# Optimization experiments

Hardware: AMD Instinct MI355X
Metric: run time of the kernel (lower is better)

## Reference

```python
import jax, jax.numpy as jnp
import numpy as np

N_NODES = 100000
N_EDGES = 3200000  # avg degree 32
D_IN = 128
D_OUT = 64
BN_EPS = 0.001


def setup_inputs() -> dict:
    key = jax.random.key(0)
    k1, k2, k3, k4, k5 = jax.random.split(key, 5)
    x = jax.random.normal(k1, (N_NODES, D_IN), dtype=jnp.float32)
    W = jax.random.normal(k2, (D_IN, D_OUT), dtype=jnp.float32) * 0.05
    edge_val = jax.random.uniform(k3, (N_EDGES,), dtype=jnp.float32)
    edge_src = jax.random.randint(k4, (N_EDGES,), 0, N_NODES, dtype=jnp.int32)
    edge_dst = jax.random.randint(k5, (N_EDGES,), 0, N_NODES, dtype=jnp.int32)
    return {"x": x, "W": W, "edge_val": edge_val,
            "edge_src": edge_src, "edge_dst": edge_dst}


def reference(x, W, edge_val, edge_src, edge_dst):
    # pre_sup = X @ W  (dense feature transform; dropout rate is 0 -> identity)
    pre_sup = x @ W  # [N, D_OUT]
    # support = A @ pre_sup, A given in COO form: A[dst, src] = edge_val
    msgs = edge_val[:, None] * pre_sup[edge_src]          # [E, D_OUT]
    out = jax.ops.segment_sum(msgs, edge_dst, num_segments=N_NODES)  # [N, D_OUT]
    # tf.nn.moments over all-but-last axis + batch_norm (no scale/offset, eps=1e-3)
    mean = jnp.mean(out, axis=0)
    var = jnp.var(out, axis=0)
    out = (out - mean) * jax.lax.rsqrt(var + BN_EPS)
    return jax.nn.relu(out)
```

## Files before the change

kernel.cpp:

```cpp
#include <hip/hip_runtime.h>
#include <stdint.h>

#define D_IN  128
#define D_OUT 64
#define BN_EPS 1e-3f

#define BIN_SHIFT 6
#define BIN_NODES 64
#define BIN_CAP   2560
#define CHUNK     8192
#define MAX_BINS  1600

typedef __attribute__((ext_vector_type(8))) short bf16x8;
typedef __attribute__((ext_vector_type(4))) float f32x4;

__device__ __forceinline__ ushort f32_to_bf16_rne(float f) {
  uint u = __float_as_uint(f);
  u += 0x7FFFu + ((u >> 16) & 1u);
  return (ushort)(u >> 16);
}
__device__ __forceinline__ float bf16_to_f32(ushort h) {
  return __uint_as_float((uint)h << 16);
}

__global__ __launch_bounds__(256) void gemm_mfma_kernel(
    const float* __restrict__ x, const float* __restrict__ W,
    ushort* __restrict__ pre16, int n_nodes, int n_tiles) {
  __shared__ ushort Wb[D_IN * D_OUT];
  const int t = threadIdx.x;
  for (int i = t; i < D_IN * D_OUT; i += 256) Wb[i] = f32_to_bf16_rne(W[i]);
  __syncthreads();

  const int lane = t & 63;
  const int wave = t >> 6;
  const int m = lane & 15;
  const int quad = lane >> 4;

  bf16x8 bfrag[4][4];
#pragma unroll
  for (int nt = 0; nt < 4; ++nt)
#pragma unroll
    for (int s = 0; s < 4; ++s)
#pragma unroll
      for (int j = 0; j < 8; ++j)
        bfrag[nt][s][j] =
            (short)Wb[(32 * s + quad * 8 + j) * D_OUT + nt * 16 + m];

  for (int tile = blockIdx.x; tile < n_tiles; tile += gridDim.x) {
    const int rbase = tile * 64 + wave * 16;
    const int row = rbase + m;
    const size_t rl = (size_t)min(row, n_nodes - 1);
    f32x4 acc0 = {0.f, 0.f, 0.f, 0.f}, acc1 = {0.f, 0.f, 0.f, 0.f};
    f32x4 acc2 = {0.f, 0.f, 0.f, 0.f}, acc3 = {0.f, 0.f, 0.f, 0.f};
#pragma unroll
    for (int s = 0; s < 4; ++s) {
      const float4 xa = *(const float4*)&x[rl * D_IN + s * 32 + quad * 8];
      const float4 xb = *(const float4*)&x[rl * D_IN + s * 32 + quad * 8 + 4];
      bf16x8 af;
      af[0] = (short)f32_to_bf16_rne(xa.x);
      af[1] = (short)f32_to_bf16_rne(xa.y);
      af[2] = (short)f32_to_bf16_rne(xa.z);
      af[3] = (short)f32_to_bf16_rne(xa.w);
      af[4] = (short)f32_to_bf16_rne(xb.x);
      af[5] = (short)f32_to_bf16_rne(xb.y);
      af[6] = (short)f32_to_bf16_rne(xb.z);
      af[7] = (short)f32_to_bf16_rne(xb.w);
      acc0 = __builtin_amdgcn_mfma_f32_16x16x32_bf16(af, bfrag[0][s], acc0, 0, 0, 0);
      acc1 = __builtin_amdgcn_mfma_f32_16x16x32_bf16(af, bfrag[1][s], acc1, 0, 0, 0);
      acc2 = __builtin_amdgcn_mfma_f32_16x16x32_bf16(af, bfrag[2][s], acc2, 0, 0, 0);
      acc3 = __builtin_amdgcn_mfma_f32_16x16x32_bf16(af, bfrag[3][s], acc3, 0, 0, 0);
    }
#pragma unroll
    for (int reg = 0; reg < 4; ++reg) {
      const int r = rbase + quad * 4 + reg;
      if (r < n_nodes) {
        ushort* po = &pre16[(size_t)r * D_OUT + m];
        po[0]  = f32_to_bf16_rne(acc0[reg]);
        po[16] = f32_to_bf16_rne(acc1[reg]);
        po[32] = f32_to_bf16_rne(acc2[reg]);
        po[48] = f32_to_bf16_rne(acc3[reg]);
      }
    }
  }
}

__global__ __launch_bounds__(256) void partition_kernel(
    const float* __restrict__ ev, const int* __restrict__ esrc,
    const int* __restrict__ edst, int* __restrict__ bin_cursor,
    uint2* __restrict__ bucket, int n_edges, int n_bins) {
  __shared__ int cnt[MAX_BINS];
  __shared__ int base[MAX_BINS];
  const int t = threadIdx.x;
  const int beg = blockIdx.x * CHUNK;
  const int end = min(beg + CHUNK, n_edges);

  for (int i = t; i < n_bins; i += 256) cnt[i] = 0;
  __syncthreads();

  for (int i = beg + t * 4; i < end; i += 1024) {
    if (i + 3 < end) {
      const int4 d4 = *(const int4*)&edst[i];
      atomicAdd(&cnt[d4.x >> BIN_SHIFT], 1);
      atomicAdd(&cnt[d4.y >> BIN_SHIFT], 1);
      atomicAdd(&cnt[d4.z >> BIN_SHIFT], 1);
      atomicAdd(&cnt[d4.w >> BIN_SHIFT], 1);
    } else {
      for (int k = i; k < end; ++k) atomicAdd(&cnt[edst[k] >> BIN_SHIFT], 1);
    }
  }
  __syncthreads();

  for (int i = t; i < n_bins; i += 256) {
    const int c = cnt[i];
    int b = 0;
    if (c > 0) b = atomicAdd(&bin_cursor[i], c);
    if (b > BIN_CAP) b = BIN_CAP;
    base[i] = i * BIN_CAP + b;
    cnt[i] = 0;
  }
  __syncthreads();

  for (int i = beg + t * 4; i < end; i += 1024) {
    if (i + 3 < end) {
      const int4 d4 = *(const int4*)&edst[i];
      const int4 s4 = *(const int4*)&esrc[i];
      const float4 v4 = *(const float4*)&ev[i];
#pragma unroll
      for (int k = 0; k < 4; ++k) {
        const int dst = (&d4.x)[k];
        const int src = (&s4.x)[k];
        const float v = (&v4.x)[k];
        const int bin = dst >> BIN_SHIFT;
        const int r = atomicAdd(&cnt[bin], 1);
        const int pos = base[bin] + r;
        if (pos < (bin + 1) * BIN_CAP) {
          const uint w0 = ((uint)(dst & (BIN_NODES - 1)) << 17) | (uint)src;
          bucket[pos] = make_uint2(w0, __float_as_uint(v));
        }
      }
    } else {
      for (int k = i; k < end; ++k) {
        const int dst = edst[k];
        const int bin = dst >> BIN_SHIFT;
        const int r = atomicAdd(&cnt[bin], 1);
        const int pos = base[bin] + r;
        if (pos < (bin + 1) * BIN_CAP) {
          const uint w0 = ((uint)(dst & (BIN_NODES - 1)) << 17) | (uint)esrc[k];
          bucket[pos] = make_uint2(w0, __float_as_uint(ev[k]));
        }
      }
    }
  }
}

__global__ __launch_bounds__(256) void bin_sort_gather_kernel(
    const ushort* __restrict__ pre16, const uint2* __restrict__ bucket,
    const int* __restrict__ bin_cursor, float* __restrict__ out,
    float* __restrict__ stats, int n_nodes) {
  __shared__ uint s_src[BIN_CAP];
  __shared__ ushort s_val[BIN_CAP];
  __shared__ int s_hist[BIN_NODES];
  __shared__ int s_off[BIN_NODES + 1];
  __shared__ int s_cur[BIN_NODES];

  const int t = threadIdx.x;
  const int bin = blockIdx.x;
  const int cnt = min(bin_cursor[bin], BIN_CAP);
  const int64_t rbase = (int64_t)bin * BIN_CAP;

  if (t < BIN_NODES) s_hist[t] = 0;
  __syncthreads();

  for (int i = t; i < cnt; i += 256)
    atomicAdd(&s_hist[bucket[rbase + i].x >> 17], 1);
  __syncthreads();

  int own = (t < BIN_NODES) ? s_hist[t] : 0;
  for (int off = 1; off < BIN_NODES; off <<= 1) {
    int u = 0;
    if (t < BIN_NODES && t >= off) u = s_hist[t - off];
    __syncthreads();
    if (t < BIN_NODES) s_hist[t] += u;
    __syncthreads();
  }
  if (t < BIN_NODES) {
    const int e = s_hist[t] - own;
    s_off[t] = e;
    s_cur[t] = e;
  }
  if (t == 0) s_off[BIN_NODES] = cnt;
  __syncthreads();

  for (int i = t; i < cnt; i += 256) {
    const uint2 r = bucket[rbase + i];
    const int d = r.x >> 17;
    const int p = atomicAdd(&s_cur[d], 1);
    s_src[p] = r.x & 0x1FFFFu;
    s_val[p] = f32_to_bf16_rne(__uint_as_float(r.y));
  }
  __syncthreads();

  const int lane = t & 63;
  const int wave = t >> 6;
  const int half = lane >> 5;
  const int hl = lane & 31;
  const int node0 = bin * BIN_NODES;
  float csx = 0.f, csy = 0.f, cs2x = 0.f, cs2y = 0.f;

  for (int nl = wave; nl < BIN_NODES; nl += 4) {
    const int node = node0 + nl;
    if (node < n_nodes) {
      const int jb = s_off[nl], je = s_off[nl + 1];
      float a0x = 0.f, a0y = 0.f, a1x = 0.f, a1y = 0.f;
      float a2x = 0.f, a2y = 0.f, a3x = 0.f, a3y = 0.f;
      float a4x = 0.f, a4y = 0.f, a5x = 0.f, a5y = 0.f;
      float a6x = 0.f, a6y = 0.f, a7x = 0.f, a7y = 0.f;
      int j = jb + half;
      for (; j + 14 < je; j += 16) {
        const uint src0 = s_src[j],      src1 = s_src[j + 2];
        const uint src2 = s_src[j + 4],  src3 = s_src[j + 6];
        const uint src4 = s_src[j + 8],  src5 = s_src[j + 10];
        const uint src6 = s_src[j + 12], src7 = s_src[j + 14];
        const float v0 = bf16_to_f32(s_val[j]);
        const float v1 = bf16_to_f32(s_val[j + 2]);
        const float v2 = bf16_to_f32(s_val[j + 4]);
        const float v3 = bf16_to_f32(s_val[j + 6]);
        const float v4 = bf16_to_f32(s_val[j + 8]);
        const float v5 = bf16_to_f32(s_val[j + 10]);
        const float v6 = bf16_to_f32(s_val[j + 12]);
        const float v7 = bf16_to_f32(s_val[j + 14]);
        const uint p0 = *(const uint*)&pre16[(size_t)src0 * D_OUT + 2 * hl];
        const uint p1 = *(const uint*)&pre16[(size_t)src1 * D_OUT + 2 * hl];
        const uint p2 = *(const uint*)&pre16[(size_t)src2 * D_OUT + 2 * hl];
        const uint p3 = *(const uint*)&pre16[(size_t)src3 * D_OUT + 2 * hl];
        const uint p4 = *(const uint*)&pre16[(size_t)src4 * D_OUT + 2 * hl];
        const uint p5 = *(const uint*)&pre16[(size_t)src5 * D_OUT + 2 * hl];
        const uint p6 = *(const uint*)&pre16[(size_t)src6 * D_OUT + 2 * hl];
        const uint p7 = *(const uint*)&pre16[(size_t)src7 * D_OUT + 2 * hl];
        a0x += v0 * bf16_to_f32((ushort)(p0 & 0xFFFFu));
        a0y += v0 * bf16_to_f32((ushort)(p0 >> 16));
        a1x += v1 * bf16_to_f32((ushort)(p1 & 0xFFFFu));
        a1y += v1 * bf16_to_f32((ushort)(p1 >> 16));
        a2x += v2 * bf16_to_f32((ushort)(p2 & 0xFFFFu));
        a2y += v2 * bf16_to_f32((ushort)(p2 >> 16));
        a3x += v3 * bf16_to_f32((ushort)(p3 & 0xFFFFu));
        a3y += v3 * bf16_to_f32((ushort)(p3 >> 16));
        a4x += v4 * bf16_to_f32((ushort)(p4 & 0xFFFFu));
        a4y += v4 * bf16_to_f32((ushort)(p4 >> 16));
        a5x += v5 * bf16_to_f32((ushort)(p5 & 0xFFFFu));
        a5y += v5 * bf16_to_f32((ushort)(p5 >> 16));
        a6x += v6 * bf16_to_f32((ushort)(p6 & 0xFFFFu));
        a6y += v6 * bf16_to_f32((ushort)(p6 >> 16));
        a7x += v7 * bf16_to_f32((ushort)(p7 & 0xFFFFu));
        a7y += v7 * bf16_to_f32((ushort)(p7 >> 16));
      }
      for (; j + 6 < je; j += 8) {
        const uint src0 = s_src[j],     src1 = s_src[j + 2];
        const uint src2 = s_src[j + 4], src3 = s_src[j + 6];
        const float v0 = bf16_to_f32(s_val[j]);
        const float v1 = bf16_to_f32(s_val[j + 2]);
        const float v2 = bf16_to_f32(s_val[j + 4]);
        const float v3 = bf16_to_f32(s_val[j + 6]);
        const uint p0 = *(const uint*)&pre16[(size_t)src0 * D_OUT + 2 * hl];
        const uint p1 = *(const uint*)&pre16[(size_t)src1 * D_OUT + 2 * hl];
        const uint p2 = *(const uint*)&pre16[(size_t)src2 * D_OUT + 2 * hl];
        const uint p3 = *(const uint*)&pre16[(size_t)src3 * D_OUT + 2 * hl];
        a0x += v0 * bf16_to_f32((ushort)(p0 & 0xFFFFu));
        a0y += v0 * bf16_to_f32((ushort)(p0 >> 16));
        a1x += v1 * bf16_to_f32((ushort)(p1 & 0xFFFFu));
        a1y += v1 * bf16_to_f32((ushort)(p1 >> 16));
        a2x += v2 * bf16_to_f32((ushort)(p2 & 0xFFFFu));
        a2y += v2 * bf16_to_f32((ushort)(p2 >> 16));
        a3x += v3 * bf16_to_f32((ushort)(p3 & 0xFFFFu));
        a3y += v3 * bf16_to_f32((ushort)(p3 >> 16));
      }
      for (; j < je; j += 2) {
        const uint src = s_src[j];
        const float v = bf16_to_f32(s_val[j]);
        const uint p = *(const uint*)&pre16[(size_t)src * D_OUT + 2 * hl];
        a0x += v * bf16_to_f32((ushort)(p & 0xFFFFu));
        a0y += v * bf16_to_f32((ushort)(p >> 16));
      }
      float ax = ((a0x + a1x) + (a2x + a3x)) + ((a4x + a5x) + (a6x + a7x));
      float ay = ((a0y + a1y) + (a2y + a3y)) + ((a4y + a5y) + (a6y + a7y));
      ax += __shfl_xor(ax, 32);
      ay += __shfl_xor(ay, 32);
      if (half == 0) {
        *(float2*)&out[(size_t)node * D_OUT + 2 * hl] = make_float2(ax, ay);
        csx += ax;
        cs2x += ax * ax;
        csy += ay;
        cs2y += ay * ay;
      }
    }
  }
  __syncthreads();

  float* red = (float*)s_src;
  float* red2 = red + 256;
  if (half == 0) {
    red[wave * 64 + 2 * hl] = csx;
    red[wave * 64 + 2 * hl + 1] = csy;
    red2[wave * 64 + 2 * hl] = cs2x;
    red2[wave * 64 + 2 * hl + 1] = cs2y;
  }
  __syncthreads();
  if (t < 64) {
    float s = red[t] + red[64 + t] + red[128 + t] + red[192 + t];
    float s2 = red2[t] + red2[64 + t] + red2[128 + t] + red2[192 + t];
    atomicAdd(&stats[t], s);
    atomicAdd(&stats[64 + t], s2);
  }
}

__global__ __launch_bounds__(256) void norm_kernel(
    float* __restrict__ out, const float* __restrict__ stats, int64_t n_vec4,
    float inv_n) {
  const int c = (threadIdx.x * 4) & 63;
  float mean[4], scale[4];
#pragma unroll
  for (int k = 0; k < 4; ++k) {
    mean[k] = stats[c + k] * inv_n;
    const float var = stats[64 + c + k] * inv_n - mean[k] * mean[k];
    scale[k] = rsqrtf(var + BN_EPS);
  }
  const int64_t stride = (int64_t)gridDim.x * 256;
  for (int64_t i = (int64_t)blockIdx.x * 256 + threadIdx.x; i < n_vec4;
       i += stride) {
    float4 v = ((float4*)out)[i];
    v.x = (v.x - mean[0]) * scale[0];
    v.y = (v.y - mean[1]) * scale[1];
    v.z = (v.z - mean[2]) * scale[2];
    v.w = (v.w - mean[3]) * scale[3];
    v.x = v.x > 0.f ? v.x : 0.f;
    v.y = v.y > 0.f ? v.y : 0.f;
    v.z = v.z > 0.f ? v.z : 0.f;
    v.w = v.w > 0.f ? v.w : 0.f;
    ((float4*)out)[i] = v;
  }
}

extern "C" void kernel_launch(void* const* d_in, const int* in_sizes, int n_in,
                              void* d_out, int out_size, void* d_ws,
                              size_t ws_size, hipStream_t stream) {
  const float* x = (const float*)d_in[0];
  const float* W = (const float*)d_in[1];
  const float* ev = (const float*)d_in[2];
  const int* esrc = (const int*)d_in[3];
  const int* edst = (const int*)d_in[4];

  const int n_nodes = in_sizes[0] / D_IN;
  const int n_edges = in_sizes[2];
  const int64_t n_out = (int64_t)n_nodes * D_OUT;
  const int n_bins = (n_nodes + BIN_NODES - 1) >> BIN_SHIFT;
  const int n_row_tiles = (n_nodes + 63) / 64;

  float* out = (float*)d_out;

  char* w = (char*)d_ws;
  ushort* pre16 = (ushort*)w;             w += (size_t)n_nodes * D_OUT * 2;
  int* bin_cursor = (int*)w;              w += (size_t)n_bins * 4;
  float* stats = (float*)w;               w += 128 * 4;
  w = (char*)(((uintptr_t)w + 7) & ~(uintptr_t)7);
  uint2* bucket = (uint2*)w;

  hipMemsetAsync(bin_cursor, 0, (size_t)n_bins * 4, stream);
  hipMemsetAsync(stats, 0, 128 * 4, stream);

  gemm_mfma_kernel<<<(n_row_tiles + 1) / 2, 256, 0, stream>>>(
      x, W, pre16, n_nodes, n_row_tiles);
  partition_kernel<<<(n_edges + CHUNK - 1) / CHUNK, 256, 0, stream>>>(
      ev, esrc, edst, bin_cursor, bucket, n_edges, n_bins);
  bin_sort_gather_kernel<<<n_bins, 256, 0, stream>>>(pre16, bucket, bin_cursor,
                                                     out, stats, n_nodes);
  norm_kernel<<<2048, 256, 0, stream>>>(out, stats, n_out / 4,
                                        1.0f / (float)n_nodes);
}
```

Before: 312.2 us.

## Split fused bin-sort/gather into separate kernels with per-node wave parallelism

The fused per-bin sort+gather kernel becomes two kernels. A bin sort kernel writes the sorted (src, val) records back to global memory along with per-node segment bounds. A gather kernel then uses one wave per node across many more blocks. BN statistic atomics are spread over 64 slices, and a small kernel reduces them, to cut atomic contention from the larger block count. The split is meant to raise occupancy and parallelism in the gather, since the old kernel's large LDS footprint limited it. The cost is an extra global round trip of the bucket data, two extra launches, and edge values kept as fp32 instead of bf16.

```diff
diff --git a/kernel.cpp b/kernel.cpp
--- a/kernel.cpp
+++ b/kernel.cpp
@@ -10,6 +10,7 @@
 #define BIN_CAP   2560
 #define CHUNK     8192
 #define MAX_BINS  1600
+#define STAT_SLICES 64
 
 typedef __attribute__((ext_vector_type(8))) short bf16x8;
 typedef __attribute__((ext_vector_type(4))) float f32x4;
@@ -153,12 +154,11 @@
   }
 }
 
-__global__ __launch_bounds__(256) void bin_sort_gather_kernel(
-    const ushort* __restrict__ pre16, const uint2* __restrict__ bucket,
-    const int* __restrict__ bin_cursor, float* __restrict__ out,
-    float* __restrict__ stats, int n_nodes) {
+__global__ __launch_bounds__(256) void bin_sort_kernel(
+    uint2* __restrict__ bucket, const int* __restrict__ bin_cursor,
+    int2* __restrict__ seg, int n_nodes) {
   __shared__ uint s_src[BIN_CAP];
-  __shared__ ushort s_val[BIN_CAP];
+  __shared__ uint s_val[BIN_CAP];
   __shared__ int s_hist[BIN_NODES];
   __shared__ int s_off[BIN_NODES + 1];
   __shared__ int s_cur[BIN_NODES];
@@ -196,108 +196,115 @@
     const int d = r.x >> 17;
     const int p = atomicAdd(&s_cur[d], 1);
     s_src[p] = r.x & 0x1FFFFu;
-    s_val[p] = f32_to_bf16_rne(__uint_as_float(r.y));
-  }
-  __syncthreads();
-
+    s_val[p] = r.y;
+  }
+  __syncthreads();
+
+  for (int i = t; i < cnt; i += 256)
+    bucket[rbase + i] = make_uint2(s_src[i], s_val[i]);
+
+  if (t < BIN_NODES) {
+    const int node = bin * BIN_NODES + t;
+    if (node < n_nodes)
+      seg[node] = make_int2((int)rbase + s_off[t], (int)rbase + s_off[t + 1]);
+  }
+}
+
+__global__ __launch_bounds__(256) void gather_kernel(
+    const ushort* __restrict__ pre16, const uint2* __restrict__ srec,
+    const int2* __restrict__ seg, float* __restrict__ out,
+    float* __restrict__ stats, int n_nodes) {
+  __shared__ float red[4 * 64];
+  __shared__ float red2[4 * 64];
+
+  const int t = threadIdx.x;
   const int lane = t & 63;
   const int wave = t >> 6;
   const int half = lane >> 5;
   const int hl = lane & 31;
-  const int node0 = bin * BIN_NODES;
+  const int node = blockIdx.x * 4 + wave;
   float csx = 0.f, csy = 0.f, cs2x = 0.f, cs2y = 0.f;
 
-  for (int nl = wave; nl < BIN_NODES; nl += 4) {
-    const int node = node0 + nl;
-    if (node < n_nodes) {
-      const int jb = s_off[nl], je = s_off[nl + 1];
-      float a0x = 0.f, a0y = 0.f, a1x = 0.f, a1y = 0.f;
-      float a2x = 0.f, a2y = 0.f, a3x = 0.f, a3y = 0.f;
-      float a4x = 0.f, a4y = 0.f, a5x = 0.f, a5y = 0.f;
-      float a6x = 0.f, a6y = 0.f, a7x = 0.f, a7y = 0.f;
-      int j = jb + half;
-      for (; j + 14 < je; j += 16) {
-        const uint src0 = s_src[j],      src1 = s_src[j + 2];
-        const uint src2 = s_src[j + 4],  src3 = s_src[j + 6];
-        const uint src4 = s_src[j + 8],  src5 = s_src[j + 10];
-        const uint src6 = s_src[j + 12], src7 = s_src[j + 14];
-        const float v0 = bf16_to_f32(s_val[j]);
-        const float v1 = bf16_to_f32(s_val[j + 2]);
-        const float v2 = bf16_to_f32(s_val[j + 4]);
-        const float v3 = bf16_to_f32(s_val[j + 6]);
-        const float v4 = bf16_to_f32(s_val[j + 8]);
-        const float v5 = bf16_to_f32(s_val[j + 10]);
-        const float v6 = bf16_to_f32(s_val[j + 12]);
-        const float v7 = bf16_to_f32(s_val[j + 14]);
-        const uint p0 = *(const uint*)&pre16[(size_t)src0 * D_OUT + 2 * hl];
-        const uint p1 = *(const uint*)&pre16[(size_t)src1 * D_OUT + 2 * hl];
-        const uint p2 = *(const uint*)&pre16[(size_t)src2 * D_OUT + 2 * hl];
-        const uint p3 = *(const uint*)&pre16[(size_t)src3 * D_OUT + 2 * hl];
-        const uint p4 = *(const uint*)&pre16[(size_t)src4 * D_OUT + 2 * hl];
-        const uint p5 = *(const uint*)&pre16[(size_t)src5 * D_OUT + 2 * hl];
-        const uint p6 = *(const uint*)&pre16[(size_t)src6 * D_OUT + 2 * hl];
-        const uint p7 = *(const uint*)&pre16[(size_t)src7 * D_OUT + 2 * hl];
-        a0x += v0 * bf16_to_f32((ushort)(p0 & 0xFFFFu));
-        a0y += v0 * bf16_to_f32((ushort)(p0 >> 16));
-        a1x += v1 * bf16_to_f32((ushort)(p1 & 0xFFFFu));
-        a1y += v1 * bf16_to_f32((ushort)(p1 >> 16));
-        a2x += v2 * bf16_to_f32((ushort)(p2 & 0xFFFFu));
-        a2y += v2 * bf16_to_f32((ushort)(p2 >> 16));
-        a3x += v3 * bf16_to_f32((ushort)(p3 & 0xFFFFu));
-        a3y += v3 * bf16_to_f32((ushort)(p3 >> 16));
-        a4x += v4 * bf16_to_f32((ushort)(p4 & 0xFFFFu));
-        a4y += v4 * bf16_to_f32((ushort)(p4 >> 16));
-        a5x += v5 * bf16_to_f32((ushort)(p5 & 0xFFFFu));
-        a5y += v5 * bf16_to_f32((ushort)(p5 >> 16));
-        a6x += v6 * bf16_to_f32((ushort)(p6 & 0xFFFFu));
-        a6y += v6 * bf16_to_f32((ushort)(p6 >> 16));
-        a7x += v7 * bf16_to_f32((ushort)(p7 & 0xFFFFu));
-        a7y += v7 * bf16_to_f32((ushort)(p7 >> 16));
-      }
-      for (; j + 6 < je; j += 8) {
-        const uint src0 = s_src[j],     src1 = s_src[j + 2];
-        const uint src2 = s_src[j + 4], src3 = s_src[j + 6];
-        const float v0 = bf16_to_f32(s_val[j]);
-        const float v1 = bf16_to_f32(s_val[j + 2]);
-        const float v2 = bf16_to_f32(s_val[j + 4]);
-        const float v3 = bf16_to_f32(s_val[j + 6]);
-        const uint p0 = *(const uint*)&pre16[(size_t)src0 * D_OUT + 2 * hl];
-        const uint p1 = *(const uint*)&pre16[(size_t)src1 * D_OUT + 2 * hl];
-        const uint p2 = *(const uint*)&pre16[(size_t)src2 * D_OUT + 2 * hl];
-        const uint p3 = *(const uint*)&pre16[(size_t)src3 * D_OUT + 2 * hl];
-        a0x += v0 * bf16_to_f32((ushort)(p0 & 0xFFFFu));
-        a0y += v0 * bf16_to_f32((ushort)(p0 >> 16));
-        a1x += v1 * bf16_to_f32((ushort)(p1 & 0xFFFFu));
-        a1y += v1 * bf16_to_f32((ushort)(p1 >> 16));
-        a2x += v2 * bf16_to_f32((ushort)(p2 & 0xFFFFu));
-        a2y += v2 * bf16_to_f32((ushort)(p2 >> 16));
-        a3x += v3 * bf16_to_f32((ushort)(p3 & 0xFFFFu));
-        a3y += v3 * bf16_to_f32((ushort)(p3 >> 16));
-      }
-      for (; j < je; j += 2) {
-        const uint src = s_src[j];
-        const float v = bf16_to_f32(s_val[j]);
-        const uint p = *(const uint*)&pre16[(size_t)src * D_OUT + 2 * hl];
-        a0x += v * bf16_to_f32((ushort)(p & 0xFFFFu));
-        a0y += v * bf16_to_f32((ushort)(p >> 16));
-      }
-      float ax = ((a0x + a1x) + (a2x + a3x)) + ((a4x + a5x) + (a6x + a7x));
-      float ay = ((a0y + a1y) + (a2y + a3y)) + ((a4y + a5y) + (a6y + a7y));
-      ax += __shfl_xor(ax, 32);
-      ay += __shfl_xor(ay, 32);
-      if (half == 0) {
-        *(float2*)&out[(size_t)node * D_OUT + 2 * hl] = make_float2(ax, ay);
-        csx += ax;
-        cs2x += ax * ax;
-        csy += ay;
-        cs2y += ay * ay;
-      }
-    }
-  }
-  __syncthreads();
-
-  float* red = (float*)s_src;
-  float* red2 = red + 256;
+  if (node < n_nodes) {
+    const int2 se = seg[node];
+    const int je = se.y;
+    float a0x = 0.f, a0y = 0.f, a1x = 0.f, a1y = 0.f;
+    float a2x = 0.f, a2y = 0.f, a3x = 0.f, a3y = 0.f;
+    float a4x = 0.f, a4y = 0.f, a5x = 0.f, a5y = 0.f;
+    float a6x = 0.f, a6y = 0.f, a7x = 0.f, a7y = 0.f;
+    int j = se.x + half;
+    for (; j + 14 < je; j += 16) {
+      const uint2 r0 = srec[j],      r1 = srec[j + 2];
+      const uint2 r2 = srec[j + 4],  r3 = srec[j + 6];
+      const uint2 r4 = srec[j + 8],  r5 = srec[j + 10];
+      const uint2 r6 = srec[j + 12], r7 = srec[j + 14];
+      const uint p0 = *(const uint*)&pre16[(size_t)r0.x * D_OUT + 2 * hl];
+      const uint p1 = *(const uint*)&pre16[(size_t)r1.x * D_OUT + 2 * hl];
+      const uint p2 = *(const uint*)&pre16[(size_t)r2.x * D_OUT + 2 * hl];
+      const uint p3 = *(const uint*)&pre16[(size_t)r3.x * D_OUT + 2 * hl];
+      const uint p4 = *(const uint*)&pre16[(size_t)r4.x * D_OUT + 2 * hl];
+      const uint p5 = *(const uint*)&pre16[(size_t)r5.x * D_OUT + 2 * hl];
+      const uint p6 = *(const uint*)&pre16[(size_t)r6.x * D_OUT + 2 * hl];
+      const uint p7 = *(const uint*)&pre16[(size_t)r7.x * D_OUT + 2 * hl];
+      const float v0 = __uint_as_float(r0.y), v1 = __uint_as_float(r1.y);
+      const float v2 = __uint_as_float(r2.y), v3 = __uint_as_float(r3.y);
+      const float v4 = __uint_as_float(r4.y), v5 = __uint_as_float(r5.y);
+      const float v6 = __uint_as_float(r6.y), v7 = __uint_as_float(r7.y);
+      a0x += v0 * bf16_to_f32((ushort)(p0 & 0xFFFFu));
+      a0y += v0 * bf16_to_f32((ushort)(p0 >> 16));
+      a1x += v1 * bf16_to_f32((ushort)(p1 & 0xFFFFu));
+      a1y += v1 * bf16_to_f32((ushort)(p1 >> 16));
+      a2x += v2 * bf16_to_f32((ushort)(p2 & 0xFFFFu));
+      a2y += v2 * bf16_to_f32((ushort)(p2 >> 16));
+      a3x += v3 * bf16_to_f32((ushort)(p3 & 0xFFFFu));
+      a3y += v3 * bf16_to_f32((ushort)(p3 >> 16));
+      a4x += v4 * bf16_to_f32((ushort)(p4 & 0xFFFFu));
+      a4y += v4 * bf16_to_f32((ushort)(p4 >> 16));
+      a5x += v5 * bf16_to_f32((ushort)(p5 & 0xFFFFu));
+      a5y += v5 * bf16_to_f32((ushort)(p5 >> 16));
+      a6x += v6 * bf16_to_f32((ushort)(p6 & 0xFFFFu));
+      a6y += v6 * bf16_to_f32((ushort)(p6 >> 16));
+      a7x += v7 * bf16_to_f32((ushort)(p7 & 0xFFFFu));
+      a7y += v7 * bf16_to_f32((ushort)(p7 >> 16));
+    }
+    for (; j + 6 < je; j += 8) {
+      const uint2 r0 = srec[j],     r1 = srec[j + 2];
+      const uint2 r2 = srec[j + 4], r3 = srec[j + 6];
+      const uint p0 = *(const uint*)&pre16[(size_t)r0.x * D_OUT + 2 * hl];
+      const uint p1 = *(const uint*)&pre16[(size_t)r1.x * D_OUT + 2 * hl];
+      const uint p2 = *(const uint*)&pre16[(size_t)r2.x * D_OUT + 2 * hl];
+      const uint p3 = *(const uint*)&pre16[(size_t)r3.x * D_OUT + 2 * hl];
+      const float v0 = __uint_as_float(r0.y), v1 = __uint_as_float(r1.y);
+      const float v2 = __uint_as_float(r2.y), v3 = __uint_as_float(r3.y);
+      a0x += v0 * bf16_to_f32((ushort)(p0 & 0xFFFFu));
+      a0y += v0 * bf16_to_f32((ushort)(p0 >> 16));
+      a1x += v1 * bf16_to_f32((ushort)(p1 & 0xFFFFu));
+      a1y += v1 * bf16_to_f32((ushort)(p1 >> 16));
+      a2x += v2 * bf16_to_f32((ushort)(p2 & 0xFFFFu));
+      a2y += v2 * bf16_to_f32((ushort)(p2 >> 16));
+      a3x += v3 * bf16_to_f32((ushort)(p3 & 0xFFFFu));
+      a3y += v3 * bf16_to_f32((ushort)(p3 >> 16));
+    }
+    for (; j < je; j += 2) {
+      const uint2 r = srec[j];
+      const float v = __uint_as_float(r.y);
+      const uint p = *(const uint*)&pre16[(size_t)r.x * D_OUT + 2 * hl];
+      a0x += v * bf16_to_f32((ushort)(p & 0xFFFFu));
+      a0y += v * bf16_to_f32((ushort)(p >> 16));
+    }
+    float ax = ((a0x + a1x) + (a2x + a3x)) + ((a4x + a5x) + (a6x + a7x));
+    float ay = ((a0y + a1y) + (a2y + a3y)) + ((a4y + a5y) + (a6y + a7y));
+    ax += __shfl_xor(ax, 32);
+    ay += __shfl_xor(ay, 32);
+    if (half == 0) {
+      *(float2*)&out[(size_t)node * D_OUT + 2 * hl] = make_float2(ax, ay);
+      csx = ax;
+      cs2x = ax * ax;
+      csy = ay;
+      cs2y = ay * ay;
+    }
+  }
+
   if (half == 0) {
     red[wave * 64 + 2 * hl] = csx;
     red[wave * 64 + 2 * hl + 1] = csy;
@@ -306,11 +313,21 @@
   }
   __syncthreads();
   if (t < 64) {
-    float s = red[t] + red[64 + t] + red[128 + t] + red[192 + t];
-    float s2 = red2[t] + red2[64 + t] + red2[128 + t] + red2[192 + t];
-    atomicAdd(&stats[t], s);
-    atomicAdd(&stats[64 + t], s2);
-  }
+    const float s = red[t] + red[64 + t] + red[128 + t] + red[192 + t];
+    const float s2 = red2[t] + red2[64 + t] + red2[128 + t] + red2[192 + t];
+    const int sl = (blockIdx.x & (STAT_SLICES - 1)) * 128;
+    atomicAdd(&stats[sl + t], s);
+    atomicAdd(&stats[sl + 64 + t], s2);
+  }
+}
+
+__global__ __launch_bounds__(128) void stats_reduce_kernel(
+    const float* __restrict__ stats, float* __restrict__ sfinal) {
+  const int c = threadIdx.x;
+  float s = 0.f;
+#pragma unroll 8
+  for (int sl = 0; sl < STAT_SLICES; ++sl) s += stats[sl * 128 + c];
+  sfinal[c] = s;
 }
 
 __global__ __launch_bounds__(256) void norm_kernel(
@@ -360,19 +377,23 @@
   char* w = (char*)d_ws;
   ushort* pre16 = (ushort*)w;             w += (size_t)n_nodes * D_OUT * 2;
   int* bin_cursor = (int*)w;              w += (size_t)n_bins * 4;
-  float* stats = (float*)w;               w += 128 * 4;
+  float* stats = (float*)w;               w += (size_t)STAT_SLICES * 128 * 4;
+  float* sfinal = (float*)w;              w += 128 * 4;
   w = (char*)(((uintptr_t)w + 7) & ~(uintptr_t)7);
+  int2* seg = (int2*)w;                   w += (size_t)n_nodes * 8;
   uint2* bucket = (uint2*)w;
 
   hipMemsetAsync(bin_cursor, 0, (size_t)n_bins * 4, stream);
-  hipMemsetAsync(stats, 0, 128 * 4, stream);
+  hipMemsetAsync(stats, 0, (size_t)STAT_SLICES * 128 * 4, stream);
 
   gemm_mfma_kernel<<<(n_row_tiles + 1) / 2, 256, 0, stream>>>(
       x, W, pre16, n_nodes, n_row_tiles);
   partition_kernel<<<(n_edges + CHUNK - 1) / CHUNK, 256, 0, stream>>>(
       ev, esrc, edst, bin_cursor, bucket, n_edges, n_bins);
-  bin_sort_gather_kernel<<<n_bins, 256, 0, stream>>>(pre16, bucket, bin_cursor,
-                                                     out, stats, n_nodes);
-  norm_kernel<<<2048, 256, 0, stream>>>(out, stats, n_out / 4,
+  bin_sort_kernel<<<n_bins, 256, 0, stream>>>(bucket, bin_cursor, seg, n_nodes);
+  gather_kernel<<<(n_nodes + 3) / 4, 256, 0, stream>>>(pre16, bucket, seg, out,
+                                                       stats, n_nodes);
+  stats_reduce_kernel<<<1, 128, 0, stream>>>(stats, sfinal);
+  norm_kernel<<<2048, 256, 0, stream>>>(out, sfinal, n_out / 4,
                                         1.0f / (float)n_nodes);
 }
```

New measurement: 316.8 us. No clear change (+1.5%).
